# Kernel tuning notes

Hardware: AMD Instinct MI355X
Metric: run time of the kernel (lower is better)

Reference implementation:

```python
import jax, jax.numpy as jnp
import numpy as np

B, N, D = 4, 1024, 1024   # batch, seq (x and context must match), model dim
H, DH = 16, 64            # heads, dim_head; inner_dim = H*DH = 1024
INNER = H * DH
EPS = 1e-5


def setup_inputs() -> dict:
    key = jax.random.key(0)
    ks = jax.random.split(key, 12)
    s = 0.02
    return {
        "x": jax.random.normal(ks[0], (B, N, D), dtype=jnp.float32),
        "context": jax.random.normal(ks[1], (B, N, D), dtype=jnp.float32),
        # weights stored as [in, out] (torch Linear weight transposed)
        "W_qk": jax.random.normal(ks[2], (D, INNER), dtype=jnp.float32) * s,
        "W_cqk": jax.random.normal(ks[3], (D, INNER), dtype=jnp.float32) * s,
        "W_v": jax.random.normal(ks[4], (D, INNER), dtype=jnp.float32) * s,
        "W_cv": jax.random.normal(ks[5], (D, INNER), dtype=jnp.float32) * s,
        "W_out": jax.random.normal(ks[6], (INNER, D), dtype=jnp.float32) * s,
        "b_out": jax.random.normal(ks[7], (D,), dtype=jnp.float32) * s,
        "W_cout": jax.random.normal(ks[8], (INNER, D), dtype=jnp.float32) * s,
        "b_cout": jax.random.normal(ks[9], (D,), dtype=jnp.float32) * s,
        "gamma": jnp.ones((D,), dtype=jnp.float32),
        "beta": jnp.zeros((D,), dtype=jnp.float32),
    }


def _split_heads(t):  # [b, n, h*d] -> [b, h, n, d]
    b, n, _ = t.shape
    return t.reshape(b, n, H, DH).transpose(0, 2, 1, 3)


def _merge_heads(t):  # [b, h, n, d] -> [b, n, h*d]
    b, h, n, d = t.shape
    return t.transpose(0, 2, 1, 3).reshape(b, n, h * d)


def _layernorm(y, gamma, beta):
    mu = jnp.mean(y, axis=-1, keepdims=True)
    var = jnp.var(y, axis=-1, keepdims=True)
    return gamma * (y - mu) * jax.lax.rsqrt(var + EPS) + beta


def reference(x, context, W_qk, W_cqk, W_v, W_cv, W_out, b_out, W_cout, b_cout, gamma, beta):
    scale = DH ** -0.5
    res = x + context                       # residual (requires identical shapes)
    # prenorm=False -> identity norms; dropout=0; talking_heads=False -> identity
    qk = _split_heads(x @ W_qk)             # [b,h,i,d]
    v = _split_heads(x @ W_v)               # [b,h,i,d]
    cqk = _split_heads(context @ W_cqk)     # [b,h,j,d]
    cv = _split_heads(context @ W_cv)       # [b,h,j,d]

    sim = jnp.einsum('bhid,bhjd->bhij', qk, cqk) * scale  # shared similarity
    attn = jax.nn.softmax(sim, axis=-1)      # row softmax (x attends to context)
    context_attn = jax.nn.softmax(sim, axis=-2)  # column softmax (context attends to x)

    out = jnp.einsum('bhij,bhjd->bhid', attn, cv)          # [b,h,i,d]
    context_out = jnp.einsum('bhji,bhjd->bhid', context_attn, v)  # [b,h,i,d]

    out = _merge_heads(out) @ W_out + b_out
    context_out = _merge_heads(context_out) @ W_cout + b_cout
    return _layernorm(out + context_out, gamma, beta) + res
```

## Files before the change

kernel.cpp:

```cpp
#include <hip/hip_runtime.h>
#include <hip/hip_bf16.h>

typedef unsigned short u16;
typedef __bf16 bf16x8 __attribute__((ext_vector_type(8)));
typedef float   f32x4 __attribute__((ext_vector_type(4)));
typedef u16     u16x8 __attribute__((ext_vector_type(8)));
typedef u16     u16x4 __attribute__((ext_vector_type(4)));

#define DEV static __device__ __forceinline__

DEV float bf2f(u16 b) { unsigned int u = ((unsigned int)b) << 16; return __builtin_bit_cast(float, u); }
DEV u16   f2bf(float f) { return __builtin_bit_cast(u16, (__bf16)f); }
DEV bf16x8 ldb(const u16* p) { return __builtin_bit_cast(bf16x8, *(const u16x8*)p); }

DEV f32x4 mfma_bf16(bf16x8 a, bf16x8 b, f32x4 c) {
  return __builtin_amdgcn_mfma_f32_16x16x32_bf16(a, b, c, 0, 0, 0);
}

DEV void gl16(const u16* g, u16* l) {
  __builtin_amdgcn_global_load_lds((const __attribute__((address_space(1))) unsigned int*)g,
                                   (__attribute__((address_space(3))) unsigned int*)l,
                                   16, 0, 0);
}

#define BAR_VM4()  asm volatile("s_waitcnt vmcnt(4)\ns_barrier" ::: "memory")
#define BAR_VM0()  asm volatile("s_waitcnt vmcnt(0)\ns_barrier" ::: "memory")
#define BAR_LG()   asm volatile("s_waitcnt lgkmcnt(0)\ns_barrier" ::: "memory")
#define BAR_FULL() asm volatile("s_waitcnt vmcnt(0) lgkmcnt(0)\ns_barrier" ::: "memory")

__global__ __launch_bounds__(256) void detect_dtype(const u16* x, int* flag) {
  int tid = threadIdx.x;
  u16 lo = x[tid * 2];
  float v = bf2f(lo);
  float av = fabsf(v);
  bool plaus = (av > 1e-4f && av < 50.f);
  __shared__ int cnt;
  if (tid == 0) cnt = 0;
  __syncthreads();
  if (plaus) atomicAdd(&cnt, 1);
  __syncthreads();
  if (tid == 0) *flag = (cnt >= 128) ? 1 : 0;
}

struct Cv2 { const void* s[2]; u16* d[2]; };
__global__ __launch_bounds__(256) void convert_big(Cv2 p, const int* flagp) {
  int fl = *flagp;
  const void* src = p.s[blockIdx.z];
  u16* dst = p.d[blockIdx.z];
  size_t i = ((size_t)blockIdx.x * 256 + threadIdx.x) * 8;
  if (fl) {
    *(u16x8*)(dst + i) = *(const u16x8*)((const u16*)src + i);
  } else {
    const float* s = (const float*)src + i;
    u16x8 o;
#pragma unroll
    for (int k = 0; k < 8; ++k) o[k] = f2bf(s[k]);
    *(u16x8*)(dst + i) = o;
  }
}

struct Sm4 { const void* s[4]; u16* d[4]; };
__global__ __launch_bounds__(256) void convert_smalls(Sm4 p, const int* flagp) {
  int fl = *flagp;
  const void* src = p.s[blockIdx.x];
  u16* dst = p.d[blockIdx.x];
  int i = threadIdx.x * 4;
#pragma unroll
  for (int k = 0; k < 4; ++k)
    dst[i + k] = fl ? ((const u16*)src)[i + k] : f2bf(((const float*)src)[i + k]);
}

struct T6 { const void* s[6]; u16* d[6]; };

__global__ __launch_bounds__(256) void transpose6(T6 t, const int* flagp) {
  int fl = *flagp;
  __shared__ u16 tile[32][33];
  const void* src = t.s[blockIdx.z];
  u16* dst = t.d[blockIdx.z];
  int x0 = blockIdx.x * 32, y0 = blockIdx.y * 32;
  int tx = threadIdx.x & 31, ty = threadIdx.x >> 5;
#pragma unroll
  for (int i = 0; i < 32; i += 8) {
    size_t idx = (size_t)(y0 + ty + i) * 1024 + x0 + tx;
    tile[ty + i][tx] = fl ? ((const u16*)src)[idx] : f2bf(((const float*)src)[idx]);
  }
  __syncthreads();
#pragma unroll
  for (int i = 0; i < 32; i += 8)
    dst[(size_t)(x0 + ty + i) * 1024 + y0 + tx] = tile[tx][ty + i];
}

struct Proj4 { const u16* A[4]; const u16* Bt[4]; u16* C[4]; int mode[4]; };

__global__ __launch_bounds__(512, 2) void gemm_proj(Proj4 p) {
  const int K = 1024, Nn = 1024;
  const u16* A  = p.A[blockIdx.z];
  const u16* Bt = p.Bt[blockIdx.z];
  u16* C = p.C[blockIdx.z];
  int mode = p.mode[blockIdx.z];

  __shared__ __align__(16) u16 As[2][256 * 64];
  __shared__ __align__(16) u16 Bs[2][256 * 64];

  int tid = threadIdx.x, lane = tid & 63, w = tid >> 6;
  int wm = w >> 2, wn = w & 3;
  int q4 = lane >> 4, c = lane & 15;

  int bid = blockIdx.y * 4 + blockIdx.x;
  int wg  = (bid & 7) * 8 + (bid >> 3);
  int m0 = (wg >> 2) * 256, n0 = (wg & 3) * 256;

  int srow = w * 8 + (lane >> 3);
  int scol = ((lane & 7) ^ (lane >> 3)) * 8;
  const u16* pAg = A  + (size_t)(m0 + srow) * K + scol;
  const u16* pBg = Bt + (size_t)(n0 + srow) * K + scol;
  int sdst = (w * 8) * 64;

  int xo0 = ((0 * 4 + q4) ^ (c & 7)) * 8;
  int xo1 = ((1 * 4 + q4) ^ (c & 7)) * 8;

  f32x4 acc[8][4] = {};

#define STAGE256(pb, kt)                                                    \
  { int ko = (kt) * 64;                                                     \
    _Pragma("unroll") for (int s = 0; s < 4; ++s) {                         \
      gl16(pAg + (size_t)s * 64 * 1024 + ko, As[pb] + s * 4096 + sdst);     \
      gl16(pBg + (size_t)s * 64 * 1024 + ko, Bs[pb] + s * 4096 + sdst);     \
    } }

#define COMP256(pb)                                                         \
  { bf16x8 bq[4][2];                                                        \
    _Pragma("unroll") for (int j = 0; j < 4; ++j) {                         \
      int rb = (wn * 64 + j * 16 + c) * 64;                                 \
      bq[j][0] = ldb(Bs[pb] + rb + xo0);                                    \
      bq[j][1] = ldb(Bs[pb] + rb + xo1);                                    \
    }                                                                       \
    _Pragma("unroll") for (int f = 0; f < 4; ++f) {                         \
      bf16x8 aq[2][2];                                                      \
      _Pragma("unroll") for (int ii = 0; ii < 2; ++ii) {                    \
        int ra = (wm * 128 + (f * 2 + ii) * 16 + c) * 64;                   \
        aq[ii][0] = ldb(As[pb] + ra + xo0);                                 \
        aq[ii][1] = ldb(As[pb] + ra + xo1);                                 \
      }                                                                     \
      __builtin_amdgcn_s_setprio(1);                                        \
      _Pragma("unroll") for (int ii = 0; ii < 2; ++ii)                      \
        _Pragma("unroll") for (int j = 0; j < 4; ++j) {                     \
          acc[f*2+ii][j] = mfma_bf16(aq[ii][0], bq[j][0], acc[f*2+ii][j]);  \
          acc[f*2+ii][j] = mfma_bf16(aq[ii][1], bq[j][1], acc[f*2+ii][j]);  \
        }                                                                   \
      __builtin_amdgcn_s_setprio(0);                                        \
    } }

  STAGE256(0, 0);
  BAR_VM0();
  for (int t = 0; t < 16; t += 2) {
    STAGE256(1, t + 1);
    COMP256(0);
    BAR_FULL();
    if (t + 2 < 16) STAGE256(0, t + 2);
    COMP256(1);
    BAR_FULL();
  }
#undef STAGE256
#undef COMP256

  if (mode == 0) {
#pragma unroll
    for (int i = 0; i < 8; ++i) {
      int mrow = m0 + wm * 128 + i * 16 + q4 * 4;
#pragma unroll
      for (int j = 0; j < 4; ++j) {
        int col = n0 + wn * 64 + j * 16 + c;
#pragma unroll
        for (int r = 0; r < 4; ++r)
          C[(size_t)(mrow + r) * Nn + col] = f2bf(acc[i][j][r]);
      }
    }
  } else {
    int bidx = m0 >> 10;
#pragma unroll
    for (int i = 0; i < 8; ++i) {
      int mrow = m0 + wm * 128 + i * 16 + q4 * 4;
      int jj = mrow & 1023;
#pragma unroll
      for (int j = 0; j < 4; ++j) {
        int col = n0 + wn * 64 + j * 16 + c;
        int h = col >> 6, dh = col & 63;
        u16x4 pk;
#pragma unroll
        for (int r = 0; r < 4; ++r) pk[r] = f2bf(acc[i][j][r]);
        *(u16x4*)(C + ((size_t)((bidx * 16 + h) * 64 + dh)) * 1024 + jj) = pk;
      }
    }
  }
}

struct FAz { const u16* Q[2]; const u16* Kp[2]; const u16* Vp[2]; u16* O[2]; };

__global__ __launch_bounds__(256) void flash_attn(FAz fa) {
  int flat = blockIdx.x;
  int i0 = (flat >> 7) * 128;
  int grp = flat & 127;
  int z = grp >> 6;
  int bh = grp & 63;
  const u16* Q  = fa.Q[z];
  const u16* Kg = fa.Kp[z];
  const u16* Vt = fa.Vp[z];
  u16* O = fa.O[z];

  int b = bh >> 4, h = bh & 15;
  int tid = threadIdx.x, lane = tid & 63, w = tid >> 6;
  int q4 = lane >> 4, c = lane & 15;

  __shared__ __align__(16) u16 Ks[64 * 64];
  __shared__ __align__(16) u16 Vs[64 * 64];
  __shared__ __align__(16) u16 Ps[4][2][16 * 72];

  bf16x8 qf[2][2];
#pragma unroll
  for (int g = 0; g < 2; ++g) {
    const size_t qoff = ((size_t)(b * 1024 + i0 + g * 64 + w * 16 + c)) * 1024 + h * 64 + q4 * 8;
    qf[g][0] = ldb(Q + qoff);
    qf[g][1] = ldb(Q + qoff + 32);
  }

  f32x4 of[2][4] = {};
  f32x4 lacc[2] = {};
  bf16x8 ones;
#pragma unroll
  for (int k = 0; k < 8; ++k) ones[k] = (__bf16)1.0f;

  int jr = tid >> 2, seg = (tid & 3) * 16;
  const u16* krow_base = Kg + ((size_t)(b * 1024 + jr)) * 1024 + h * 64 + seg;
  const u16* vrow_base = Vt + ((size_t)((b * 16 + h) * 64 + jr)) * 1024 + seg;

  int ch0 = (tid & 3) * 2, jrx = jr & 7;
  int wa0 = jr * 64 + ((ch0)     ^ jrx) * 8;
  int wa1 = jr * 64 + ((ch0 + 1) ^ jrx) * 8;
  int xA = (q4 ^ (c & 7)) * 8;
  int xB = xA ^ 32;

  const float C2 = 0.125f * 1.4426950408889634f;

  u16x8 kv0 = *(const u16x8*)(krow_base);
  u16x8 kv1 = *(const u16x8*)(krow_base + 8);
  u16x8 vv0 = *(const u16x8*)(vrow_base);
  u16x8 vv1 = *(const u16x8*)(vrow_base + 8);

  for (int j0 = 0; j0 < 1024; j0 += 64) {
    __syncthreads();
    *(u16x8*)(Ks + wa0) = kv0;
    *(u16x8*)(Ks + wa1) = kv1;
    *(u16x8*)(Vs + wa0) = vv0;
    *(u16x8*)(Vs + wa1) = vv1;
    __syncthreads();

    if (j0 + 64 < 1024) {
      const u16* ks = krow_base + (size_t)(j0 + 64) * 1024;
      kv0 = *(const u16x8*)(ks);
      kv1 = *(const u16x8*)(ks + 8);
      const u16* vs = vrow_base + j0 + 64;
      vv0 = *(const u16x8*)(vs);
      vv1 = *(const u16x8*)(vs + 8);
    }

    f32x4 sf[2][4] = {};
    __builtin_amdgcn_s_setprio(1);
#pragma unroll
    for (int jc = 0; jc < 4; ++jc) {
      int rk = (jc * 16 + c) * 64;
      bf16x8 k0f = ldb(Ks + rk + xA);
      bf16x8 k1f = ldb(Ks + rk + xB);
#pragma unroll
      for (int g = 0; g < 2; ++g) {
        sf[g][jc] = mfma_bf16(k0f, qf[g][0], sf[g][jc]);
        sf[g][jc] = mfma_bf16(k1f, qf[g][1], sf[g][jc]);
      }
    }
    __builtin_amdgcn_s_setprio(0);

#pragma unroll
    for (int g = 0; g < 2; ++g)
#pragma unroll
      for (int jc = 0; jc < 4; ++jc) {
        u16x4 pk;
#pragma unroll
        for (int r = 0; r < 4; ++r)
          pk[r] = f2bf(__builtin_amdgcn_exp2f(sf[g][jc][r] * C2));
        *(u16x4*)(Ps[w][g] + c * 72 + jc * 16 + q4 * 4) = pk;
      }

    asm volatile("s_waitcnt lgkmcnt(0)" ::: "memory");

    bf16x8 pf[2][2];
#pragma unroll
    for (int g = 0; g < 2; ++g) {
      pf[g][0] = ldb(Ps[w][g] + c * 72 + q4 * 8);
      pf[g][1] = ldb(Ps[w][g] + c * 72 + 32 + q4 * 8);
      lacc[g] = mfma_bf16(pf[g][0], ones, lacc[g]);
      lacc[g] = mfma_bf16(pf[g][1], ones, lacc[g]);
    }

    __builtin_amdgcn_s_setprio(1);
#pragma unroll
    for (int dc = 0; dc < 4; ++dc) {
      int rv = (dc * 16 + c) * 64;
      bf16x8 v0f = ldb(Vs + rv + xA);
      bf16x8 v1f = ldb(Vs + rv + xB);
#pragma unroll
      for (int g = 0; g < 2; ++g) {
        of[g][dc] = mfma_bf16(pf[g][0], v0f, of[g][dc]);
        of[g][dc] = mfma_bf16(pf[g][1], v1f, of[g][dc]);
      }
    }
    __builtin_amdgcn_s_setprio(0);
  }

#pragma unroll
  for (int g = 0; g < 2; ++g) {
    float inv[4];
#pragma unroll
    for (int r = 0; r < 4; ++r) inv[r] = 1.0f / lacc[g][r];
#pragma unroll
    for (int dc = 0; dc < 4; ++dc) {
      int col = h * 64 + dc * 16 + c;
#pragma unroll
      for (int r = 0; r < 4; ++r) {
        int irow = i0 + g * 64 + w * 16 + q4 * 4 + r;
        O[((size_t)(b * 1024 + irow)) * 1024 + col] = f2bf(of[g][dc][r] * inv[r]);
      }
    }
  }
}

__global__ __launch_bounds__(256) void gemm_final(const u16* A1, const u16* B1t,
                                                  const u16* A2, const u16* B2t,
                                                  const u16* b1, const u16* b2,
                                                  float* Y) {
  const int K = 1024, Nn = 1024;
  __shared__ __align__(16) u16 As[2][128 * 32];
  __shared__ __align__(16) u16 Bs[2][128 * 32];

  int tid = threadIdx.x, lane = tid & 63, w = tid >> 6;
  int wm = w & 1, wn = w >> 1;
  int q4 = lane >> 4, c = lane & 15;

  int bid = blockIdx.y * 8 + blockIdx.x;
  int wg  = (bid & 7) * 32 + (bid >> 3);
  int m0 = (wg >> 3) * 128, n0 = (wg & 7) * 128;

  int r0 = w * 32 + (lane >> 2);
  int cc = (lane & 3) ^ ((lane >> 3) & 3);
  const u16* A1p = A1  + (size_t)(m0 + r0) * K + cc * 8;
  const u16* A2p = A2  + (size_t)(m0 + r0) * K + cc * 8;
  const u16* B1p = B1t + (size_t)(n0 + r0) * K + cc * 8;
  const u16* B2p = B2t + (size_t)(n0 + r0) * K + cc * 8;
  int qs = (q4 ^ ((c >> 1) & 3)) * 8;

  f32x4 acc[4][4] = {};

#define STAGE_F(buf, kk)                                          \
  { const u16* Ap = ((kk) < 32) ? A1p : A2p;                      \
    const u16* Bp = ((kk) < 32) ? B1p : B2p;                      \
    int k0_ = ((kk) & 31) * 32;                                   \
    gl16(Ap + k0_,          As[buf] + w * 1024);                  \
    gl16(Ap + 16 * K + k0_, As[buf] + w * 1024 + 512);            \
    gl16(Bp + k0_,          Bs[buf] + w * 1024);                  \
    gl16(Bp + 16 * K + k0_, Bs[buf] + w * 1024 + 512); }

#define COMP_F(buf)                                               \
  { bf16x8 af[4], bfr[4];                                         \
    _Pragma("unroll") for (int i = 0; i < 4; ++i)                 \
      af[i]  = ldb(As[buf] + (wm * 64 + i * 16 + c) * 32 + qs);   \
    _Pragma("unroll") for (int j = 0; j < 4; ++j)                 \
      bfr[j] = ldb(Bs[buf] + (wn * 64 + j * 16 + c) * 32 + qs);   \
    _Pragma("unroll") for (int i = 0; i < 4; ++i)                 \
      _Pragma("unroll") for (int j = 0; j < 4; ++j)               \
        acc[i][j] = mfma_bf16(af[i], bfr[j], acc[i][j]); }

  STAGE_F(0, 0);
  for (int t = 0; t < 62; t += 2) {
    STAGE_F(1, t + 1);
    BAR_VM4();
    COMP_F(0);
    BAR_LG();
    STAGE_F(0, t + 2);
    BAR_VM4();
    COMP_F(1);
    BAR_LG();
  }
  STAGE_F(1, 63);
  BAR_VM4();
  COMP_F(0);
  BAR_LG();
  BAR_VM0();
  COMP_F(1);
#undef STAGE_F
#undef COMP_F

#pragma unroll
  for (int i = 0; i < 4; ++i) {
    int mrow = m0 + wm * 64 + i * 16 + q4 * 4;
#pragma unroll
    for (int j = 0; j < 4; ++j) {
      int col = n0 + wn * 64 + j * 16 + c;
      float bias = bf2f(b1[col]) + bf2f(b2[col]);
#pragma unroll
      for (int r = 0; r < 4; ++r)
        Y[(size_t)(mrow + r) * Nn + col] = acc[i][j][r] + bias;
    }
  }
}

__global__ __launch_bounds__(256) void ln_res(const float* Y, const u16* gamma, const u16* beta,
                                              const void* x, const void* ctx, void* out,
                                              const int* flagp) {
  int fl = *flagp;
  int row = blockIdx.x;
  int tid = threadIdx.x;
  const float* y = Y + (size_t)row * 1024;
  float4 v = *(const float4*)(y + tid * 4);
  float s  = v.x + v.y + v.z + v.w;
  float s2 = v.x * v.x + v.y * v.y + v.z * v.z + v.w * v.w;
#pragma unroll
  for (int off = 1; off < 64; off <<= 1) { s += __shfl_xor(s, off); s2 += __shfl_xor(s2, off); }
  __shared__ float red[8];
  int w = tid >> 6, lane = tid & 63;
  if (lane == 0) { red[w] = s; red[w + 4] = s2; }
  __syncthreads();
  float S  = red[0] + red[1] + red[2] + red[3];
  float S2 = red[4] + red[5] + red[6] + red[7];
  float mu  = S * (1.0f / 1024.0f);
  float var = S2 * (1.0f / 1024.0f) - mu * mu;
  float rs = rsqrtf(var + 1e-5f);
  size_t base = (size_t)row * 1024 + tid * 4;
  u16x4 gv = *(const u16x4*)(gamma + tid * 4);
  u16x4 bv = *(const u16x4*)(beta + tid * 4);
  float xr[4], cr[4];
  if (fl) {
    u16x4 xv = *(const u16x4*)((const u16*)x + base);
    u16x4 cv = *(const u16x4*)((const u16*)ctx + base);
#pragma unroll
    for (int k = 0; k < 4; ++k) { xr[k] = bf2f(xv[k]); cr[k] = bf2f(cv[k]); }
  } else {
    float4 xv = *(const float4*)((const float*)x + base);
    float4 cv = *(const float4*)((const float*)ctx + base);
    xr[0] = xv.x; xr[1] = xv.y; xr[2] = xv.z; xr[3] = xv.w;
    cr[0] = cv.x; cr[1] = cv.y; cr[2] = cv.z; cr[3] = cv.w;
  }
  float vv[4] = {v.x, v.y, v.z, v.w};
  float o[4];
#pragma unroll
  for (int k = 0; k < 4; ++k)
    o[k] = bf2f(gv[k]) * (vv[k] - mu) * rs + bf2f(bv[k]) + xr[k] + cr[k];
  if (fl) {
    u16x4 ov;
#pragma unroll
    for (int k = 0; k < 4; ++k) ov[k] = f2bf(o[k]);
    *(u16x4*)((u16*)out + base) = ov;
  } else {
    *(float4*)((float*)out + base) = make_float4(o[0], o[1], o[2], o[3]);
  }
}

__global__ __launch_bounds__(256) void sentinel(u16* out) {
  size_t i = ((size_t)blockIdx.x * 256 + threadIdx.x) * 8;
  u16 v = f2bf(12345.0f);
  u16x8 o = {v, v, v, v, v, v, v, v};
  *(u16x8*)(out + i) = o;
}

extern "C" void kernel_launch(void* const* d_in, const int* in_sizes, int n_in,
                              void* d_out, int out_size, void* d_ws, size_t ws_size,
                              hipStream_t stream) {
  (void)in_sizes; (void)n_in; (void)out_size;
  const size_t MB = 1024 * 1024;
  const size_t NEED = 61 * MB;
  if (ws_size < NEED) {
    sentinel<<<2048, 256, 0, stream>>>((u16*)d_out);
    return;
  }

  char* ws = (char*)d_ws;
  u16* wt[6];
  for (int i = 0; i < 6; ++i) wt[i] = (u16*)(ws + (size_t)i * 2 * MB);
  u16* xc   = (u16*)(ws + 12 * MB);
  u16* cc   = (u16*)(ws + 20 * MB);
  u16* qk   = (u16*)(ws + 28 * MB);
  u16* cqk  = (u16*)(ws + 36 * MB);
  u16* vt   = (u16*)(ws + 44 * MB);
  u16* cvt  = (u16*)(ws + 52 * MB);
  u16* oa   = (u16*)(ws + 0);
  u16* ca   = (u16*)(ws + 12 * MB);
  float* y  = (float*)(ws + 28 * MB);
  int* flag = (int*)(ws + 60 * MB);
  u16* b1c  = (u16*)(ws + 60 * MB + 4096);
  u16* b2c  = (u16*)(ws + 60 * MB + 8192);
  u16* gc   = (u16*)(ws + 60 * MB + 12288);
  u16* bc   = (u16*)(ws + 60 * MB + 16384);

  detect_dtype<<<1, 256, 0, stream>>>((const u16*)d_in[0], flag);

  Cv2 cv;
  cv.s[0] = d_in[0]; cv.d[0] = xc;
  cv.s[1] = d_in[1]; cv.d[1] = cc;
  convert_big<<<dim3(2048, 1, 2), 256, 0, stream>>>(cv, flag);

  Sm4 sm;
  sm.s[0] = d_in[7]; sm.d[0] = b1c;
  sm.s[1] = d_in[9]; sm.d[1] = b2c;
  sm.s[2] = d_in[10]; sm.d[2] = gc;
  sm.s[3] = d_in[11]; sm.d[3] = bc;
  convert_smalls<<<4, 256, 0, stream>>>(sm, flag);

  T6 t;
  t.s[0] = d_in[2]; t.d[0] = wt[0];
  t.s[1] = d_in[3]; t.d[1] = wt[1];
  t.s[2] = d_in[4]; t.d[2] = wt[2];
  t.s[3] = d_in[5]; t.d[3] = wt[3];
  t.s[4] = d_in[6]; t.d[4] = wt[4];
  t.s[5] = d_in[8]; t.d[5] = wt[5];
  transpose6<<<dim3(32, 32, 6), 256, 0, stream>>>(t, flag);

  Proj4 p;
  p.A[0] = xc; p.Bt[0] = wt[0]; p.C[0] = qk;  p.mode[0] = 0;
  p.A[1] = cc; p.Bt[1] = wt[1]; p.C[1] = cqk; p.mode[1] = 0;
  p.A[2] = xc; p.Bt[2] = wt[2]; p.C[2] = vt;  p.mode[2] = 1;
  p.A[3] = cc; p.Bt[3] = wt[3]; p.C[3] = cvt; p.mode[3] = 1;
  gemm_proj<<<dim3(4, 16, 4), 512, 0, stream>>>(p);

  FAz fa;
  fa.Q[0] = qk;  fa.Kp[0] = cqk; fa.Vp[0] = cvt; fa.O[0] = oa;
  fa.Q[1] = cqk; fa.Kp[1] = qk;  fa.Vp[1] = vt;  fa.O[1] = ca;
  flash_attn<<<dim3(1024), 256, 0, stream>>>(fa);

  gemm_final<<<dim3(8, 32), 256, 0, stream>>>(oa, wt[4], ca, wt[5], b1c, b2c, y);

  ln_res<<<4096, 256, 0, stream>>>(y, gc, bc, d_in[0], d_in[1], d_out, flag);
}
```

Measured before the change: 259.2 us.

## Enlarge flash-attention query tile and gemm_final tile to 256x256 with 512 threads

The attention kernel now gives each block 256 query rows instead of 128, so each K/V tile loaded into shared memory is reused across twice as many queries, with half as many blocks. The final output GEMM moves to 256x256 tiles with a 64-wide K step, 8 waves and a new XOR-swizzled LDS layout, aiming for more data reuse per load. In exchange there is much higher register pressure (more accumulators), fewer blocks to fill the GPU (only 64 GEMM blocks and 512 attention blocks), and full barriers in the GEMM loop that serialise loads and compute.

```diff
diff --git a/kernel.cpp b/kernel.cpp
--- a/kernel.cpp
+++ b/kernel.cpp
@@ -23,9 +23,7 @@
                                    16, 0, 0);
 }
 
-#define BAR_VM4()  asm volatile("s_waitcnt vmcnt(4)\ns_barrier" ::: "memory")
 #define BAR_VM0()  asm volatile("s_waitcnt vmcnt(0)\ns_barrier" ::: "memory")
-#define BAR_LG()   asm volatile("s_waitcnt lgkmcnt(0)\ns_barrier" ::: "memory")
 #define BAR_FULL() asm volatile("s_waitcnt vmcnt(0) lgkmcnt(0)\ns_barrier" ::: "memory")
 
 __global__ __launch_bounds__(256) void detect_dtype(const u16* x, int* flag) {
@@ -199,7 +197,7 @@
 
 __global__ __launch_bounds__(256) void flash_attn(FAz fa) {
   int flat = blockIdx.x;
-  int i0 = (flat >> 7) * 128;
+  int i0 = (flat >> 7) * 256;
   int grp = flat & 127;
   int z = grp >> 6;
   int bh = grp & 63;
@@ -214,18 +212,18 @@
 
   __shared__ __align__(16) u16 Ks[64 * 64];
   __shared__ __align__(16) u16 Vs[64 * 64];
-  __shared__ __align__(16) u16 Ps[4][2][16 * 72];
-
-  bf16x8 qf[2][2];
-#pragma unroll
-  for (int g = 0; g < 2; ++g) {
+  __shared__ __align__(16) u16 Ps[4][4][16 * 72];
+
+  bf16x8 qf[4][2];
+#pragma unroll
+  for (int g = 0; g < 4; ++g) {
     const size_t qoff = ((size_t)(b * 1024 + i0 + g * 64 + w * 16 + c)) * 1024 + h * 64 + q4 * 8;
     qf[g][0] = ldb(Q + qoff);
     qf[g][1] = ldb(Q + qoff + 32);
   }
 
-  f32x4 of[2][4] = {};
-  f32x4 lacc[2] = {};
+  f32x4 of[4][4] = {};
+  f32x4 lacc[4] = {};
   bf16x8 ones;
 #pragma unroll
   for (int k = 0; k < 8; ++k) ones[k] = (__bf16)1.0f;
@@ -264,7 +262,7 @@
       vv1 = *(const u16x8*)(vs + 8);
     }
 
-    f32x4 sf[2][4] = {};
+    f32x4 sf[4][4] = {};
     __builtin_amdgcn_s_setprio(1);
 #pragma unroll
     for (int jc = 0; jc < 4; ++jc) {
@@ -272,7 +270,7 @@
       bf16x8 k0f = ldb(Ks + rk + xA);
       bf16x8 k1f = ldb(Ks + rk + xB);
 #pragma unroll
-      for (int g = 0; g < 2; ++g) {
+      for (int g = 0; g < 4; ++g) {
         sf[g][jc] = mfma_bf16(k0f, qf[g][0], sf[g][jc]);
         sf[g][jc] = mfma_bf16(k1f, qf[g][1], sf[g][jc]);
       }
@@ -280,7 +278,7 @@
     __builtin_amdgcn_s_setprio(0);
 
 #pragma unroll
-    for (int g = 0; g < 2; ++g)
+    for (int g = 0; g < 4; ++g)
 #pragma unroll
       for (int jc = 0; jc < 4; ++jc) {
         u16x4 pk;
@@ -292,9 +290,9 @@
 
     asm volatile("s_waitcnt lgkmcnt(0)" ::: "memory");
 
-    bf16x8 pf[2][2];
-#pragma unroll
-    for (int g = 0; g < 2; ++g) {
+    bf16x8 pf[4][2];
+#pragma unroll
+    for (int g = 0; g < 4; ++g) {
       pf[g][0] = ldb(Ps[w][g] + c * 72 + q4 * 8);
       pf[g][1] = ldb(Ps[w][g] + c * 72 + 32 + q4 * 8);
       lacc[g] = mfma_bf16(pf[g][0], ones, lacc[g]);
@@ -308,7 +306,7 @@
       bf16x8 v0f = ldb(Vs + rv + xA);
       bf16x8 v1f = ldb(Vs + rv + xB);
 #pragma unroll
-      for (int g = 0; g < 2; ++g) {
+      for (int g = 0; g < 4; ++g) {
         of[g][dc] = mfma_bf16(pf[g][0], v0f, of[g][dc]);
         of[g][dc] = mfma_bf16(pf[g][1], v1f, of[g][dc]);
       }
@@ -317,7 +315,7 @@
   }
 
 #pragma unroll
-  for (int g = 0; g < 2; ++g) {
+  for (int g = 0; g < 4; ++g) {
     float inv[4];
 #pragma unroll
     for (int r = 0; r < 4; ++r) inv[r] = 1.0f / lacc[g][r];
@@ -333,74 +331,83 @@
   }
 }
 
-__global__ __launch_bounds__(256) void gemm_final(const u16* A1, const u16* B1t,
-                                                  const u16* A2, const u16* B2t,
-                                                  const u16* b1, const u16* b2,
-                                                  float* Y) {
+__global__ __launch_bounds__(512, 2) void gemm_final(const u16* A1, const u16* B1t,
+                                                     const u16* A2, const u16* B2t,
+                                                     const u16* b1, const u16* b2,
+                                                     float* Y) {
   const int K = 1024, Nn = 1024;
-  __shared__ __align__(16) u16 As[2][128 * 32];
-  __shared__ __align__(16) u16 Bs[2][128 * 32];
+  __shared__ __align__(16) u16 As[2][256 * 64];
+  __shared__ __align__(16) u16 Bs[2][256 * 64];
 
   int tid = threadIdx.x, lane = tid & 63, w = tid >> 6;
-  int wm = w & 1, wn = w >> 1;
+  int wm = w >> 2, wn = w & 3;
   int q4 = lane >> 4, c = lane & 15;
 
-  int bid = blockIdx.y * 8 + blockIdx.x;
-  int wg  = (bid & 7) * 32 + (bid >> 3);
-  int m0 = (wg >> 3) * 128, n0 = (wg & 7) * 128;
-
-  int r0 = w * 32 + (lane >> 2);
-  int cc = (lane & 3) ^ ((lane >> 3) & 3);
-  const u16* A1p = A1  + (size_t)(m0 + r0) * K + cc * 8;
-  const u16* A2p = A2  + (size_t)(m0 + r0) * K + cc * 8;
-  const u16* B1p = B1t + (size_t)(n0 + r0) * K + cc * 8;
-  const u16* B2p = B2t + (size_t)(n0 + r0) * K + cc * 8;
-  int qs = (q4 ^ ((c >> 1) & 3)) * 8;
-
-  f32x4 acc[4][4] = {};
-
-#define STAGE_F(buf, kk)                                          \
-  { const u16* Ap = ((kk) < 32) ? A1p : A2p;                      \
-    const u16* Bp = ((kk) < 32) ? B1p : B2p;                      \
-    int k0_ = ((kk) & 31) * 32;                                   \
-    gl16(Ap + k0_,          As[buf] + w * 1024);                  \
-    gl16(Ap + 16 * K + k0_, As[buf] + w * 1024 + 512);            \
-    gl16(Bp + k0_,          Bs[buf] + w * 1024);                  \
-    gl16(Bp + 16 * K + k0_, Bs[buf] + w * 1024 + 512); }
-
-#define COMP_F(buf)                                               \
-  { bf16x8 af[4], bfr[4];                                         \
-    _Pragma("unroll") for (int i = 0; i < 4; ++i)                 \
-      af[i]  = ldb(As[buf] + (wm * 64 + i * 16 + c) * 32 + qs);   \
-    _Pragma("unroll") for (int j = 0; j < 4; ++j)                 \
-      bfr[j] = ldb(Bs[buf] + (wn * 64 + j * 16 + c) * 32 + qs);   \
-    _Pragma("unroll") for (int i = 0; i < 4; ++i)                 \
-      _Pragma("unroll") for (int j = 0; j < 4; ++j)               \
-        acc[i][j] = mfma_bf16(af[i], bfr[j], acc[i][j]); }
-
-  STAGE_F(0, 0);
-  for (int t = 0; t < 62; t += 2) {
-    STAGE_F(1, t + 1);
-    BAR_VM4();
-    COMP_F(0);
-    BAR_LG();
-    STAGE_F(0, t + 2);
-    BAR_VM4();
-    COMP_F(1);
-    BAR_LG();
-  }
-  STAGE_F(1, 63);
-  BAR_VM4();
-  COMP_F(0);
-  BAR_LG();
+  int bid = blockIdx.y * 4 + blockIdx.x;
+  int wg  = (bid & 7) * 8 + (bid >> 3);
+  int m0 = (wg >> 2) * 256, n0 = (wg & 3) * 256;
+
+  int srow = w * 8 + (lane >> 3);
+  int scol = ((lane & 7) ^ (lane >> 3)) * 8;
+  const u16* pA1 = A1  + (size_t)(m0 + srow) * K + scol;
+  const u16* pA2 = A2  + (size_t)(m0 + srow) * K + scol;
+  const u16* pB1 = B1t + (size_t)(n0 + srow) * K + scol;
+  const u16* pB2 = B2t + (size_t)(n0 + srow) * K + scol;
+  int sdst = (w * 8) * 64;
+
+  int xo0 = ((0 * 4 + q4) ^ (c & 7)) * 8;
+  int xo1 = ((1 * 4 + q4) ^ (c & 7)) * 8;
+
+  f32x4 acc[8][4] = {};
+
+#define STAGE_FIN(pb, kt)                                                   \
+  { const u16* Ap = ((kt) < 16) ? pA1 : pA2;                                \
+    const u16* Bp = ((kt) < 16) ? pB1 : pB2;                                \
+    int ko = ((kt) & 15) * 64;                                              \
+    _Pragma("unroll") for (int s = 0; s < 4; ++s) {                         \
+      gl16(Ap + (size_t)s * 64 * 1024 + ko, As[pb] + s * 4096 + sdst);      \
+      gl16(Bp + (size_t)s * 64 * 1024 + ko, Bs[pb] + s * 4096 + sdst);      \
+    } }
+
+#define COMP_FIN(pb)                                                        \
+  { bf16x8 bq[4][2];                                                        \
+    _Pragma("unroll") for (int j = 0; j < 4; ++j) {                         \
+      int rb = (wn * 64 + j * 16 + c) * 64;                                 \
+      bq[j][0] = ldb(Bs[pb] + rb + xo0);                                    \
+      bq[j][1] = ldb(Bs[pb] + rb + xo1);                                    \
+    }                                                                       \
+    _Pragma("unroll") for (int f = 0; f < 4; ++f) {                         \
+      bf16x8 aq[2][2];                                                      \
+      _Pragma("unroll") for (int ii = 0; ii < 2; ++ii) {                    \
+        int ra = (wm * 128 + (f * 2 + ii) * 16 + c) * 64;                   \
+        aq[ii][0] = ldb(As[pb] + ra + xo0);                                 \
+        aq[ii][1] = ldb(As[pb] + ra + xo1);                                 \
+      }                                                                     \
+      __builtin_amdgcn_s_setprio(1);                                        \
+      _Pragma("unroll") for (int ii = 0; ii < 2; ++ii)                      \
+        _Pragma("unroll") for (int j = 0; j < 4; ++j) {                     \
+          acc[f*2+ii][j] = mfma_bf16(aq[ii][0], bq[j][0], acc[f*2+ii][j]);  \
+          acc[f*2+ii][j] = mfma_bf16(aq[ii][1], bq[j][1], acc[f*2+ii][j]);  \
+        }                                                                   \
+      __builtin_amdgcn_s_setprio(0);                                        \
+    } }
+
+  STAGE_FIN(0, 0);
   BAR_VM0();
-  COMP_F(1);
-#undef STAGE_F
-#undef COMP_F
-
-#pragma unroll
-  for (int i = 0; i < 4; ++i) {
-    int mrow = m0 + wm * 64 + i * 16 + q4 * 4;
+  for (int t = 0; t < 32; t += 2) {
+    STAGE_FIN(1, t + 1);
+    COMP_FIN(0);
+    BAR_FULL();
+    if (t + 2 < 32) STAGE_FIN(0, t + 2);
+    COMP_FIN(1);
+    BAR_FULL();
+  }
+#undef STAGE_FIN
+#undef COMP_FIN
+
+#pragma unroll
+  for (int i = 0; i < 8; ++i) {
+    int mrow = m0 + wm * 128 + i * 16 + q4 * 4;
 #pragma unroll
     for (int j = 0; j < 4; ++j) {
       int col = n0 + wn * 64 + j * 16 + c;
@@ -532,9 +539,9 @@
   FAz fa;
   fa.Q[0] = qk;  fa.Kp[0] = cqk; fa.Vp[0] = cvt; fa.O[0] = oa;
   fa.Q[1] = cqk; fa.Kp[1] = qk;  fa.Vp[1] = vt;  fa.O[1] = ca;
-  flash_attn<<<dim3(1024), 256, 0, stream>>>(fa);
-
-  gemm_final<<<dim3(8, 32), 256, 0, stream>>>(oa, wt[4], ca, wt[5], b1c, b2c, y);
+  flash_attn<<<dim3(512), 256, 0, stream>>>(fa);
+
+  gemm_final<<<dim3(4, 16), 512, 0, stream>>>(oa, wt[4], ca, wt[5], b1c, b2c, y);
 
   ln_res<<<4096, 256, 0, stream>>>(y, gc, bc, d_in[0], d_in[1], d_out, flag);
 }
```

Measured after the change: 282.9 us. 9.1% more time.
